# Kernel tuning notes

Hardware: AMD Instinct MI355X
Metric: run time of the kernel (lower is better)

The kernel has to match this reference:

```python
import jax, jax.numpy as jnp
import numpy as np

HEADS = 4
BN_EPS = 1e-5


def setup_inputs() -> dict:
    key = jax.random.key(0)
    k1, k2, k3 = jax.random.split(key, 3)
    b, c, n = 4, 256, 4096
    x = jax.random.normal(k1, (b, c, n), dtype=jnp.float32)
    bn_weight = jnp.ones((c,), dtype=jnp.float32)
    bn_bias = jnp.zeros((c,), dtype=jnp.float32)
    # 1x1 Conv1d kernels are plain [out, in] matrices
    w_qkv = jax.random.normal(k2, (3 * c, c), dtype=jnp.float32) * (c ** -0.5)
    w_out = jax.random.normal(k3, (c, c), dtype=jnp.float32) * (c ** -0.5)
    b_out = jnp.zeros((c,), dtype=jnp.float32)
    return {"x": x, "bn_weight": bn_weight, "bn_bias": bn_bias,
            "w_qkv": w_qkv, "w_out": w_out, "b_out": b_out}


def reference(x, bn_weight, bn_bias, w_qkv, w_out, b_out):
    b, c, n = x.shape
    h = HEADS
    d = c // h
    scale = d ** -0.5

    # BatchNorm1d (training-mode batch statistics over batch and length dims)
    mean = jnp.mean(x, axis=(0, 2), keepdims=True)            # [1,c,1]
    var = jnp.var(x, axis=(0, 2), keepdims=True)
    xn = (x - mean) * jax.lax.rsqrt(var + BN_EPS)
    xn = xn * bn_weight[None, :, None] + bn_bias[None, :, None]

    # 1x1 conv QKV projection == matmul over channel dim
    qkv = jnp.einsum('oc,bcn->bon', w_qkv, xn)                # [b,3c,n]
    q, k, v = jnp.split(qkv, 3, axis=1)                       # each [b,c,n]
    # b (h d) n -> b h d n
    q = q.reshape(b, h, d, n) * scale
    k = k.reshape(b, h, d, n)
    v = v.reshape(b, h, d, n)

    attn = jax.nn.softmax(jnp.einsum('bhdi,bhdj->bhij', q, k), axis=-1)
    out = jnp.einsum('bhij,bhdj->bhid', attn, v)              # [b,h,n,d]
    # b h n d -> b (h d) n
    out = out.transpose(0, 1, 3, 2).reshape(b, c, n)
    return jnp.einsum('oc,bcn->bon', w_out, out) + b_out[None, :, None]
```

## Files before the change

### kernel.cpp

```cpp
#include <hip/hip_runtime.h>
#include <stdint.h>

#define B_ 4
#define C_ 256
#define N_ 4096
#define H_ 4
#define DH_ 64
#define BH_ 16
#define NTH 32

typedef __bf16 bf16x8 __attribute__((ext_vector_type(8)));
typedef float  f32x4  __attribute__((ext_vector_type(4)));
typedef float  f32x16 __attribute__((ext_vector_type(16)));
typedef unsigned short u16;

__device__ __forceinline__ u16 f2bf(float f) {
  uint32_t u = __float_as_uint(f);
  return (u16)((u + 0x7FFFu + ((u >> 16) & 1u)) >> 16);
}
__device__ __forceinline__ f32x4 mfma16(bf16x8 a, bf16x8 b, f32x4 c) {
  return __builtin_amdgcn_mfma_f32_16x16x32_bf16(a, b, c, 0, 0, 0);
}
__device__ __forceinline__ f32x16 mfma32(bf16x8 a, bf16x8 b, f32x16 c) {
  return __builtin_amdgcn_mfma_f32_32x32x16_bf16(a, b, c, 0, 0, 0);
}
__device__ __forceinline__ unsigned pk2(float a, float b) {
  unsigned r;
  asm("v_cvt_pk_bf16_f32 %0, %1, %2" : "=v"(r) : "v"(a), "v"(b));
  return r;
}
__device__ __forceinline__ float max3f(float a, float b, float c) {
  float r;
  asm("v_max3_f32 %0, %1, %2, %3" : "=v"(r) : "v"(a), "v"(b), "v"(c));
  return r;
}

__global__ __launch_bounds__(256) void k_bnstats(const float* __restrict__ x,
    const float* __restrict__ bw, const float* __restrict__ bbias,
    float* __restrict__ a, float* __restrict__ bb) {
  int ch = blockIdx.x, t = threadIdx.x;
  float s1 = 0.f, s2 = 0.f;
  for (int b = 0; b < B_; ++b) {
    const float4* p = (const float4*)(x + ((size_t)b * C_ + ch) * N_);
    for (int i = t; i < N_ / 4; i += 256) {
      float4 v = p[i];
      s1 += v.x + v.y + v.z + v.w;
      s2 += v.x * v.x + v.y * v.y + v.z * v.z + v.w * v.w;
    }
  }
  for (int off = 32; off; off >>= 1) { s1 += __shfl_down(s1, off); s2 += __shfl_down(s2, off); }
  __shared__ float r1[4], r2[4];
  int w = t >> 6;
  if ((t & 63) == 0) { r1[w] = s1; r2[w] = s2; }
  __syncthreads();
  if (t == 0) {
    s1 = r1[0] + r1[1] + r1[2] + r1[3];
    s2 = r2[0] + r2[1] + r2[2] + r2[3];
    const float inv = 1.f / (B_ * N_);
    float mean = s1 * inv;
    float var  = s2 * inv - mean * mean;
    float av = bw[ch] * rsqrtf(var + 1e-5f);
    a[ch] = av;
    bb[ch] = bbias[ch] - mean * av;
  }
}

__global__ __launch_bounds__(256) void k_fold(const float* __restrict__ wq,
    const float* __restrict__ wo, const float* __restrict__ a, const float* __restrict__ bb,
    u16* __restrict__ wqf, float* __restrict__ qb, u16* __restrict__ woh) {
  int o = blockIdx.x, t = threadIdx.x;
  if (o < 3 * C_) {
    float w = wq[o * C_ + t];
    wqf[o * C_ + t] = f2bf(w * a[t]);
    float contrib = w * bb[t];
    for (int off = 32; off; off >>= 1) contrib += __shfl_down(contrib, off);
    __shared__ float r[4];
    if ((t & 63) == 0) r[t >> 6] = contrib;
    __syncthreads();
    if (t == 0) qb[o] = r[0] + r[1] + r[2] + r[3];
  } else {
    int oo = o - 3 * C_;
    woh[oo * C_ + t] = f2bf(wo[oo * C_ + t]);
  }
}

__global__ __launch_bounds__(256) void k_transpose(const float* __restrict__ x,
                                                   u16* __restrict__ xT) {
  __shared__ float tile[64][65];
  int nb = blockIdx.x * 64, cb = blockIdx.y * 64, b = blockIdx.z;
  int t = threadIdx.x;
  int col = t & 63, rq = t >> 6;
  #pragma unroll
  for (int it = 0; it < 16; ++it) {
    int r = it * 4 + rq;
    tile[r][col] = x[((size_t)b * C_ + cb + r) * N_ + nb + col];
  }
  __syncthreads();
  #pragma unroll
  for (int it = 0; it < 16; ++it) {
    int r = it * 4 + rq;
    xT[((size_t)b * N_ + nb + r) * C_ + cb + col] = f2bf(tile[col][r]);
  }
}

__global__ __launch_bounds__(256) void k_qkvgemm(const u16* __restrict__ xT,
    const u16* __restrict__ wqf, const float* __restrict__ qb,
    u16* __restrict__ q, u16* __restrict__ kk, u16* __restrict__ vtt) {
  __shared__ __align__(16) u16 As[128 * 64];
  __shared__ __align__(16) u16 Bs[128 * 64];
  int b = blockIdx.y;
  int bx = blockIdx.x;
  int mt = bx % 32, ot = bx / 32;
  int mbase = mt * 128, obase = ot * 128;
  int tid = threadIdx.x, w = tid >> 6, lane = tid & 63, lg = lane >> 4, lr = lane & 15;
  int wm = w >> 1, wn = w & 1;
  f32x4 acc[4][4] = {};
  const char* asrc = (const char*)xT + ((size_t)b * N_ + mbase) * 512;
  const char* bsrc = (const char*)wqf + (size_t)obase * 512;

  for (int ks = 0; ks < 4; ++ks) {
    int kbase = ks * 64;
    #pragma unroll
    for (int rr = 0; rr < 4; ++rr) {
      int p = tid * 16 + rr * 4096;
      int row = p >> 7, col = p & 127;
      int phys = p ^ ((row & 7) << 4);
      *(bf16x8*)((char*)As + phys) = *(const bf16x8*)(asrc + (size_t)row * 512 + kbase * 2 + col);
      *(bf16x8*)((char*)Bs + phys) = *(const bf16x8*)(bsrc + (size_t)row * 512 + kbase * 2 + col);
    }
    __syncthreads();
    #pragma unroll
    for (int kc = 0; kc < 2; ++kc) {
      bf16x8 af[4], bfr[4];
      #pragma unroll
      for (int i = 0; i < 4; ++i) {
        int r = wm * 64 + i * 16 + lr;
        int L = r * 128 + kc * 64 + lg * 16;
        af[i] = *(const bf16x8*)((const char*)As + (L ^ ((r & 7) << 4)));
        int rb = wn * 64 + i * 16 + lr;
        int Lb = rb * 128 + kc * 64 + lg * 16;
        bfr[i] = *(const bf16x8*)((const char*)Bs + (Lb ^ ((rb & 7) << 4)));
      }
      #pragma unroll
      for (int i = 0; i < 4; ++i)
        #pragma unroll
        for (int jj = 0; jj < 4; ++jj)
          acc[i][jj] = mfma16(af[i], bfr[jj], acc[i][jj]);
    }
    __syncthreads();
  }

  int s_id = (obase + wn * 64) >> 8;
  int h = ((obase + wn * 64) >> 6) & 3;
  int bh = b * H_ + h;
  float scale = (s_id == 0) ? 0.18033688011112042f : 1.f;
  #pragma unroll
  for (int i = 0; i < 4; ++i) {
    int n0 = mbase + wm * 64 + i * 16 + lg * 4;
    #pragma unroll
    for (int jj = 0; jj < 4; ++jj) {
      int o = obase + wn * 64 + jj * 16 + lr;
      int dd = jj * 16 + lr;
      float bias = qb[o];
      if (s_id == 2) {
        ushort4 pk;
        pk.x = f2bf(acc[i][jj][0] + bias);
        pk.y = f2bf(acc[i][jj][1] + bias);
        pk.z = f2bf(acc[i][jj][2] + bias);
        pk.w = f2bf(acc[i][jj][3] + bias);
        *(ushort4*)(vtt + ((size_t)bh * DH_ + dd) * N_ + n0) = pk;
      } else {
        u16* dst = (s_id == 0 ? q : kk) + (size_t)bh * N_ * DH_;
        #pragma unroll
        for (int r2 = 0; r2 < 4; ++r2)
          dst[(size_t)(n0 + r2) * DH_ + dd] = f2bf((acc[i][jj][r2] + bias) * scale);
      }
    }
  }
}

#define AS1 __attribute__((address_space(1)))
#define AS3 __attribute__((address_space(3)))

__global__ __launch_bounds__(256, 4) void k_attn(const u16* __restrict__ q,
    const u16* __restrict__ k, const u16* __restrict__ vt,
    u16* __restrict__ O0, u16* __restrict__ O1, float* __restrict__ lse) {
  __shared__ __align__(16) char kt_s[2][8192];
  __shared__ __align__(16) char vt_s[2][8192];
  int id = blockIdx.x;
  int xcd = id & 7, j = id >> 3;
  int bh = xcd * 2 + (j >> 6);
  int rem = j & 63;
  int qbase = (rem >> 1) * 128;
  int half = rem & 1;
  int tid = threadIdx.x, w = tid >> 6, lane = tid & 63;
  int l31 = lane & 31, hi = lane >> 5;

  const char* kg = (const char*)(k + ((size_t)bh * N_ + half * 2048) * DH_);
  const char* vg = (const char*)(vt + (size_t)bh * DH_ * N_ + half * 2048);

  int poff0 = w * 2048 + lane * 16;
  int poff1 = poff0 + 1024;
  int L0 = poff0 ^ (((poff0 >> 7) & 7) << 4);
  int L1 = poff1 ^ (((poff1 >> 7) & 7) << 4);
  const char* ks0 = kg + L0;
  const char* ks1 = kg + L1;
  const char* vs0 = vg + (size_t)(L0 >> 7) * 8192 + (L0 & 127);
  const char* vs1 = vg + (size_t)(L1 >> 7) * 8192 + (L1 & 127);

  bf16x8 bq[4];
  {
    const u16* qp = q + ((size_t)bh * N_ + qbase + w * 32 + l31) * DH_;
    #pragma unroll
    for (int cc = 0; cc < 4; ++cc)
      bq[cc] = *(const bf16x8*)(qp + cc * 16 + hi * 8);
  }

  f32x16 Oacc0, Oacc1;
  #pragma unroll
  for (int i = 0; i < 16; ++i) { Oacc0[i] = 0.f; Oacc1[i] = 0.f; }
  float m = 0.f, l = 0.f;

  auto stage = [&](int par) {
    __builtin_amdgcn_global_load_lds((const AS1 void*)ks0,
        (AS3 void*)(kt_s[par] + w * 2048), 16, 0, 0);
    __builtin_amdgcn_global_load_lds((const AS1 void*)ks1,
        (AS3 void*)(kt_s[par] + w * 2048 + 1024), 16, 0, 0);
    __builtin_amdgcn_global_load_lds((const AS1 void*)vs0,
        (AS3 void*)(vt_s[par] + w * 2048), 16, 0, 0);
    __builtin_amdgcn_global_load_lds((const AS1 void*)vs1,
        (AS3 void*)(vt_s[par] + w * 2048 + 1024), 16, 0, 0);
    ks0 += 8192; ks1 += 8192; vs0 += 128; vs1 += 128;
  };

  auto body = [&](int kt, int par) {
    __syncthreads();
    if (kt + 1 < NTH) stage(par ^ 1);

    const char* kb = (const char*)kt_s[par];
    const char* vb = (const char*)vt_s[par];
    int vsw = (l31 & 7) << 4;
    int rb0 = l31 * 128;
    int rb1 = rb0 + 4096;

    f32x16 s0, s1;
    float negm = -m;
    #pragma unroll
    for (int i = 0; i < 16; ++i) { s0[i] = negm; s1[i] = negm; }
    __builtin_amdgcn_s_setprio(1);
    #pragma unroll
    for (int cc = 0; cc < 4; ++cc) {
      bf16x8 kf0 = *(const bf16x8*)(kb + ((rb0 + cc * 32 + hi * 16) ^ vsw));
      bf16x8 kf1 = *(const bf16x8*)(kb + ((rb1 + cc * 32 + hi * 16) ^ vsw));
      s0 = mfma32(kf0, bq[cc], s0);
      s1 = mfma32(kf1, bq[cc], s1);
    }
    __builtin_amdgcn_s_setprio(0);

    float a0 = max3f(s0[0], s0[1], s0[2]);
    float a1 = max3f(s0[3], s0[4], s0[5]);
    float a2 = max3f(s0[6], s0[7], s0[8]);
    float a3 = max3f(s0[9], s0[10], s0[11]);
    float a4 = max3f(s0[12], s0[13], max3f(s0[14], s0[15], s1[0]));
    float a5 = max3f(s1[1], s1[2], s1[3]);
    float a6 = max3f(s1[4], s1[5], s1[6]);
    float a7 = max3f(s1[7], s1[8], s1[9]);
    float a8 = max3f(s1[10], s1[11], s1[12]);
    float a9 = max3f(s1[13], s1[14], s1[15]);
    float b0 = max3f(a0, a1, a2);
    float b1 = max3f(a3, a4, a5);
    float b2 = max3f(a6, a7, a8);
    float mxloc = max3f(b0, b1, max3f(b2, a9, a9));

    if (!__all(mxloc <= 8.f)) {
      float mx = fmaxf(mxloc, __shfl_xor(mxloc, 32));
      float delta = fmaxf(mx, 0.f);
      float al = __builtin_amdgcn_exp2f(-delta);
      m += delta; l *= al;
      #pragma unroll
      for (int i = 0; i < 16; ++i) { s0[i] -= delta; s1[i] -= delta; }
      #pragma unroll
      for (int i = 0; i < 16; ++i) { Oacc0[i] *= al; Oacc1[i] *= al; }
    }

    #pragma unroll
    for (int i = 0; i < 16; ++i) s0[i] = __builtin_amdgcn_exp2f(s0[i]);
    {
      float u0 = s0[0] + s0[1], u1 = s0[2] + s0[3], u2 = s0[4] + s0[5], u3 = s0[6] + s0[7];
      float u4 = s0[8] + s0[9], u5 = s0[10] + s0[11], u6 = s0[12] + s0[13], u7 = s0[14] + s0[15];
      l += ((u0 + u1) + (u2 + u3)) + ((u4 + u5) + (u6 + u7));
    }
    #pragma unroll
    for (int kslot = 0; kslot < 2; ++kslot) {
      const int a8i = kslot * 8;
      unsigned p0 = pk2(s0[a8i + 0], s0[a8i + 1]);
      unsigned p1 = pk2(s0[a8i + 2], s0[a8i + 3]);
      unsigned p2 = pk2(s0[a8i + 4], s0[a8i + 5]);
      unsigned p3 = pk2(s0[a8i + 6], s0[a8i + 7]);
      asm("v_permlane32_swap_b32 %0, %1" : "+v"(p0), "+v"(p2));
      asm("v_permlane32_swap_b32 %0, %1" : "+v"(p1), "+v"(p3));
      union { unsigned u[4]; bf16x8 b; } cv;
      cv.u[0] = p0; cv.u[1] = p1; cv.u[2] = p2; cv.u[3] = p3;
      bf16x8 pa = cv.b;
      int colb = kslot * 32 + hi * 16;
      __builtin_amdgcn_s_setprio(1);
      {
        bf16x8 vf = *(const bf16x8*)(vb + ((rb0 + colb) ^ vsw));
        Oacc0 = mfma32(vf, pa, Oacc0);
      }
      {
        bf16x8 vf = *(const bf16x8*)(vb + ((rb1 + colb) ^ vsw));
        Oacc1 = mfma32(vf, pa, Oacc1);
      }
      __builtin_amdgcn_s_setprio(0);
    }

    #pragma unroll
    for (int i = 0; i < 16; ++i) s1[i] = __builtin_amdgcn_exp2f(s1[i]);
    {
      float u0 = s1[0] + s1[1], u1 = s1[2] + s1[3], u2 = s1[4] + s1[5], u3 = s1[6] + s1[7];
      float u4 = s1[8] + s1[9], u5 = s1[10] + s1[11], u6 = s1[12] + s1[13], u7 = s1[14] + s1[15];
      l += ((u0 + u1) + (u2 + u3)) + ((u4 + u5) + (u6 + u7));
    }
    #pragma unroll
    for (int kslot = 0; kslot < 2; ++kslot) {
      const int a8i = kslot * 8;
      unsigned p0 = pk2(s1[a8i + 0], s1[a8i + 1]);
      unsigned p1 = pk2(s1[a8i + 2], s1[a8i + 3]);
      unsigned p2 = pk2(s1[a8i + 4], s1[a8i + 5]);
      unsigned p3 = pk2(s1[a8i + 6], s1[a8i + 7]);
      asm("v_permlane32_swap_b32 %0, %1" : "+v"(p0), "+v"(p2));
      asm("v_permlane32_swap_b32 %0, %1" : "+v"(p1), "+v"(p3));
      union { unsigned u[4]; bf16x8 b; } cv;
      cv.u[0] = p0; cv.u[1] = p1; cv.u[2] = p2; cv.u[3] = p3;
      bf16x8 pa = cv.b;
      int colb = 64 + kslot * 32 + hi * 16;
      __builtin_amdgcn_s_setprio(1);
      {
        bf16x8 vf = *(const bf16x8*)(vb + ((rb0 + colb) ^ vsw));
        Oacc0 = mfma32(vf, pa, Oacc0);
      }
      {
        bf16x8 vf = *(const bf16x8*)(vb + ((rb1 + colb) ^ vsw));
        Oacc1 = mfma32(vf, pa, Oacc1);
      }
      __builtin_amdgcn_s_setprio(0);
    }
  };

  stage(0);
  for (int kt = 0; kt < NTH; kt += 2) {
    body(kt, 0);
    body(kt + 1, 1);
  }

  l += __shfl_xor(l, 32);
  float rl = 1.f / l;
  float lse_v = m + __builtin_amdgcn_logf(l);
  int qrow = qbase + w * 32 + l31;
  u16* dst = (half ? O1 : O0) + ((size_t)bh * N_ + qrow) * DH_;
  #pragma unroll
  for (int dt = 0; dt < 2; ++dt) {
    const f32x16& O = dt ? Oacc1 : Oacc0;
    #pragma unroll
    for (int rq = 0; rq < 4; ++rq) {
      ushort4 pk4;
      pk4.x = f2bf(O[rq * 4 + 0] * rl);
      pk4.y = f2bf(O[rq * 4 + 1] * rl);
      pk4.z = f2bf(O[rq * 4 + 2] * rl);
      pk4.w = f2bf(O[rq * 4 + 3] * rl);
      *(ushort4*)(dst + dt * 32 + rq * 8 + hi * 4) = pk4;
    }
  }
  if (hi == 0) lse[half * (BH_ * N_) + bh * N_ + qrow] = lse_v;
}

__global__ __launch_bounds__(256) void k_outgemm(const u16* __restrict__ O0,
    const u16* __restrict__ O1, const float* __restrict__ lse,
    const u16* __restrict__ woh, const float* __restrict__ b_out,
    float* __restrict__ out) {
  __shared__ __align__(16) u16 As[128 * 64];
  __shared__ __align__(16) u16 Bs[128 * 64];
  int b = blockIdx.y;
  int bx = blockIdx.x;
  int mt = bx & 31, ot = bx >> 5;
  int mbase = mt * 128, obase = ot * 128;
  int tid = threadIdx.x, w = tid >> 6, lane = tid & 63, lg = lane >> 4, lr = lane & 15;
  int wm = w >> 1, wn = w & 1;
  f32x4 acc[4][4] = {};
  const char* bsrc = (const char*)woh + (size_t)obase * 512;

  for (int ks = 0; ks < 4; ++ks) {
    int kbase = ks * 64;
    int h = kbase >> 6;
    int bh = b * H_ + h;
    const char* a0 = (const char*)O0 + ((size_t)bh * N_ + mbase) * 128;
    const char* a1 = (const char*)O1 + ((size_t)bh * N_ + mbase) * 128;
    const float* lp0 = lse + (size_t)bh * N_ + mbase;
    const float* lp1 = lp0 + (size_t)BH_ * N_;
    #pragma unroll
    for (int rr = 0; rr < 4; ++rr) {
      int p = tid * 16 + rr * 4096;
      int row = p >> 7, col = p & 127;
      int phys = p ^ ((row & 7) << 4);
      float e0 = lp0[row], e1 = lp1[row];
      float Mx = fmaxf(e0, e1);
      float w0 = __builtin_amdgcn_exp2f(e0 - Mx);
      float w1 = __builtin_amdgcn_exp2f(e1 - Mx);
      float inv = 1.f / (w0 + w1);
      w0 *= inv; w1 *= inv;
      uint4 av = *(const uint4*)(a0 + p);
      uint4 bv = *(const uint4*)(a1 + p);
      uint4 o;
      #pragma unroll
      for (int i = 0; i < 4; ++i) {
        unsigned ua = (&av.x)[i], ub = (&bv.x)[i];
        float alo = __uint_as_float(ua << 16), ahi = __uint_as_float(ua & 0xFFFF0000u);
        float blo = __uint_as_float(ub << 16), bhi = __uint_as_float(ub & 0xFFFF0000u);
        (&o.x)[i] = pk2(w0 * alo + w1 * blo, w0 * ahi + w1 * bhi);
      }
      *(uint4*)((char*)As + phys) = o;
      *(bf16x8*)((char*)Bs + phys) = *(const bf16x8*)(bsrc + (size_t)row * 512 + kbase * 2 + col);
    }
    __syncthreads();
    #pragma unroll
    for (int kc = 0; kc < 2; ++kc) {
      bf16x8 af[4], bfr[4];
      #pragma unroll
      for (int i = 0; i < 4; ++i) {
        int r = wm * 64 + i * 16 + lr;
        int L = r * 128 + kc * 64 + lg * 16;
        af[i] = *(const bf16x8*)((const char*)As + (L ^ ((r & 7) << 4)));
        int rb = wn * 64 + i * 16 + lr;
        int Lb = rb * 128 + kc * 64 + lg * 16;
        bfr[i] = *(const bf16x8*)((const char*)Bs + (Lb ^ ((rb & 7) << 4)));
      }
      #pragma unroll
      for (int i = 0; i < 4; ++i)
        #pragma unroll
        for (int jj = 0; jj < 4; ++jj)
          acc[i][jj] = mfma16(af[i], bfr[jj], acc[i][jj]);
    }
    __syncthreads();
  }

  #pragma unroll
  for (int i = 0; i < 4; ++i) {
    int n0 = mbase + wm * 64 + i * 16 + lg * 4;
    #pragma unroll
    for (int jj = 0; jj < 4; ++jj) {
      int o = obase + wn * 64 + jj * 16 + lr;
      float bias = b_out[o];
      float4 vv = make_float4(acc[i][jj][0] + bias, acc[i][jj][1] + bias,
                              acc[i][jj][2] + bias, acc[i][jj][3] + bias);
      *(float4*)(out + ((size_t)(b * C_ + o)) * N_ + n0) = vv;
    }
  }
}

extern "C" void kernel_launch(void* const* d_in, const int* in_sizes, int n_in,
                              void* d_out, int out_size, void* d_ws, size_t ws_size,
                              hipStream_t stream) {
  const float* x    = (const float*)d_in[0];
  const float* bnw  = (const float*)d_in[1];
  const float* bnb  = (const float*)d_in[2];
  const float* wqkv = (const float*)d_in[3];
  const float* wout = (const float*)d_in[4];
  const float* bout = (const float*)d_in[5];
  float* out = (float*)d_out;
  char* ws = (char*)d_ws;

  float* a   = (float*)(ws + 0);
  float* bb  = (float*)(ws + 1024);
  float* qb  = (float*)(ws + 2048);
  u16* wqf = (u16*)(ws + 8192);
  u16* woh = (u16*)(ws + 8192 + 393216);
  const size_t big = 8388608;
  u16* xT  = (u16*)(ws + 532480);
  u16* q   = (u16*)(ws + 532480 + 1 * big);
  u16* kk  = (u16*)(ws + 532480 + 2 * big);
  u16* vt  = (u16*)(ws + 532480 + 3 * big);
  u16* O0  = (u16*)(ws + 532480 + 4 * big);
  float* lse = (float*)(ws + 532480 + 5 * big);

  k_bnstats <<<256, 256, 0, stream>>>(x, bnw, bnb, a, bb);
  k_fold    <<<1024, 256, 0, stream>>>(wqkv, wout, a, bb, wqf, qb, woh);
  k_transpose<<<dim3(64, 4, 4), 256, 0, stream>>>(x, xT);
  k_qkvgemm <<<dim3(192, 4), 256, 0, stream>>>(xT, wqf, qb, q, kk, vt);
  k_attn    <<<dim3(1024), 256, 0, stream>>>(q, kk, vt, O0, xT, lse);
  k_outgemm <<<dim3(64, 4), 256, 0, stream>>>(O0, xT, lse, woh, bout, out);
}
```

Before: 143.8 us.

## Fuse BatchNorm statistics into transpose kernel and add small finalize reduction

Computes per-channel partial sums and sums of squares inside the transpose kernel from the already-loaded shared tile, writing 1024 partials per channel into reused workspace. A new small kernel reduces the partials into the BN scale/shift. This removes a separate full pass over the fp32 input for statistics, at the cost of an extra launch and partial-buffer traffic.

Measured after the change: 142.5 us. No clear change (-0.9%).

```diff
diff --git a/kernel.cpp b/kernel.cpp
--- a/kernel.cpp
+++ b/kernel.cpp
@@ -35,23 +35,48 @@
   return r;
 }
 
-__global__ __launch_bounds__(256) void k_bnstats(const float* __restrict__ x,
-    const float* __restrict__ bw, const float* __restrict__ bbias,
-    float* __restrict__ a, float* __restrict__ bb) {
+__global__ __launch_bounds__(256) void k_transpose(const float* __restrict__ x,
+    u16* __restrict__ xT, float* __restrict__ s1p, float* __restrict__ s2p) {
+  __shared__ float tile[64][65];
+  int nbt = blockIdx.x, nb = nbt * 64, cb = blockIdx.y * 64, b = blockIdx.z;
+  int t = threadIdx.x;
+  int col = t & 63, rq = t >> 6;
+  #pragma unroll
+  for (int it = 0; it < 16; ++it) {
+    int r = it * 4 + rq;
+    tile[r][col] = x[((size_t)b * C_ + cb + r) * N_ + nb + col];
+  }
+  __syncthreads();
+  #pragma unroll
+  for (int it = 0; it < 16; ++it) {
+    int r = it * 4 + rq;
+    xT[((size_t)b * N_ + nb + r) * C_ + cb + col] = f2bf(tile[col][r]);
+  }
+  float s1 = 0.f, s2 = 0.f;
+  #pragma unroll
+  for (int i = 0; i < 16; ++i) {
+    float v = tile[col][rq * 16 + i];
+    s1 += v;
+    s2 = fmaf(v, v, s2);
+  }
+  int part = (b * 64 + nbt) * 4 + rq;
+  s1p[(size_t)(cb + col) * 1024 + part] = s1;
+  s2p[(size_t)(cb + col) * 1024 + part] = s2;
+}
+
+__global__ __launch_bounds__(256) void k_bnfin(const float* __restrict__ s1p,
+    const float* __restrict__ s2p, const float* __restrict__ bw,
+    const float* __restrict__ bbias, float* __restrict__ a, float* __restrict__ bb) {
   int ch = blockIdx.x, t = threadIdx.x;
   float s1 = 0.f, s2 = 0.f;
-  for (int b = 0; b < B_; ++b) {
-    const float4* p = (const float4*)(x + ((size_t)b * C_ + ch) * N_);
-    for (int i = t; i < N_ / 4; i += 256) {
-      float4 v = p[i];
-      s1 += v.x + v.y + v.z + v.w;
-      s2 += v.x * v.x + v.y * v.y + v.z * v.z + v.w * v.w;
-    }
-  }
-  for (int off = 32; off; off >>= 1) { s1 += __shfl_down(s1, off); s2 += __shfl_down(s2, off); }
+  #pragma unroll
+  for (int i = 0; i < 4; ++i) {
+    s1 += s1p[(size_t)ch * 1024 + i * 256 + t];
+    s2 += s2p[(size_t)ch * 1024 + i * 256 + t];
+  }
+  for (int off = 32; off; off >>= 1) { s1 += __shfl_xor(s1, off); s2 += __shfl_xor(s2, off); }
   __shared__ float r1[4], r2[4];
-  int w = t >> 6;
-  if ((t & 63) == 0) { r1[w] = s1; r2[w] = s2; }
+  if ((t & 63) == 0) { r1[t >> 6] = s1; r2[t >> 6] = s2; }
   __syncthreads();
   if (t == 0) {
     s1 = r1[0] + r1[1] + r1[2] + r1[3];
@@ -84,25 +109,6 @@
   }
 }
 
-__global__ __launch_bounds__(256) void k_transpose(const float* __restrict__ x,
-                                                   u16* __restrict__ xT) {
-  __shared__ float tile[64][65];
-  int nb = blockIdx.x * 64, cb = blockIdx.y * 64, b = blockIdx.z;
-  int t = threadIdx.x;
-  int col = t & 63, rq = t >> 6;
-  #pragma unroll
-  for (int it = 0; it < 16; ++it) {
-    int r = it * 4 + rq;
-    tile[r][col] = x[((size_t)b * C_ + cb + r) * N_ + nb + col];
-  }
-  __syncthreads();
-  #pragma unroll
-  for (int it = 0; it < 16; ++it) {
-    int r = it * 4 + rq;
-    xT[((size_t)b * N_ + nb + r) * C_ + cb + col] = f2bf(tile[col][r]);
-  }
-}
-
 __global__ __launch_bounds__(256) void k_qkvgemm(const u16* __restrict__ xT,
     const u16* __restrict__ wqf, const float* __restrict__ qb,
     u16* __restrict__ q, u16* __restrict__ kk, u16* __restrict__ vtt) {
@@ -482,10 +488,12 @@
   u16* vt  = (u16*)(ws + 532480 + 3 * big);
   u16* O0  = (u16*)(ws + 532480 + 4 * big);
   float* lse = (float*)(ws + 532480 + 5 * big);
-
-  k_bnstats <<<256, 256, 0, stream>>>(x, bnw, bnb, a, bb);
+  float* s1p = (float*)(ws + 532480 + 1 * big);
+  float* s2p = (float*)(ws + 532480 + 1 * big + 1048576);
+
+  k_transpose<<<dim3(64, 4, 4), 256, 0, stream>>>(x, xT, s1p, s2p);
+  k_bnfin   <<<256, 256, 0, stream>>>(s1p, s2p, bnw, bnb, a, bb);
   k_fold    <<<1024, 256, 0, stream>>>(wqkv, wout, a, bb, wqf, qb, woh);
-  k_transpose<<<dim3(64, 4, 4), 256, 0, stream>>>(x, xT);
   k_qkvgemm <<<dim3(192, 4), 256, 0, stream>>>(xT, wqf, qb, q, kk, vt);
   k_attn    <<<dim3(1024), 256, 0, stream>>>(q, kk, vt, O0, xT, lse);
   k_outgemm <<<dim3(64, 4), 256, 0, stream>>>(O0, xT, lse, woh, bout, out);
```
